# Kernel tuning notes

Measured on AMD Instinct MI355X. Metric: run time of the kernel, lower is better.

## Reference

```python
import jax, jax.numpy as jnp
import numpy as np

B, T, D_IN = 32, 1024, 80
SHAPES = (512, 512, 256)
WIN = 2          # delta window
H = 256          # LSTM hidden units (per direction)
LSTM_IN = SHAPES[-1] * 3


def setup_inputs() -> dict:
    key = jax.random.key(0)
    ks = jax.random.split(key, 20)
    inp = {}
    inp["x"] = jax.random.normal(ks[0], (B, T, D_IN), dtype=jnp.float32)
    lens = jax.random.randint(ks[1], (B,), T // 2, T + 1)
    inp["x_lengths"] = lens.at[0].set(T)  # ensure max length == T (static output shape)
    dims = (D_IN,) + SHAPES
    for i in range(len(SHAPES)):
        s = 1.0 / np.sqrt(dims[i])
        inp[f"enc_W{i}"] = jax.random.uniform(ks[2 + i], (dims[i + 1], dims[i]), minval=-s, maxval=s, dtype=jnp.float32)
        inp[f"enc_b{i}"] = jax.random.uniform(ks[5 + i], (dims[i + 1],), minval=-s, maxval=s, dtype=jnp.float32)
    s = 1.0 / np.sqrt(H)
    for d, name in enumerate(("f", "b")):
        inp[f"W_ih_{name}"] = jax.random.uniform(ks[8 + 4 * d], (4 * H, LSTM_IN), minval=-s, maxval=s, dtype=jnp.float32)
        inp[f"W_hh_{name}"] = jax.random.uniform(ks[9 + 4 * d], (4 * H, H), minval=-s, maxval=s, dtype=jnp.float32)
        inp[f"b_ih_{name}"] = jax.random.uniform(ks[10 + 4 * d], (4 * H,), minval=-s, maxval=s, dtype=jnp.float32)
        inp[f"b_hh_{name}"] = jax.random.uniform(ks[11 + 4 * d], (4 * H,), minval=-s, maxval=s, dtype=jnp.float32)
    # init_hidden() in torch uses randn; fix it here as deterministic inputs. [2 dirs, B, H]
    inp["h0"] = jax.random.normal(ks[16], (2, B, H), dtype=jnp.float32)
    inp["c0"] = jax.random.normal(ks[17], (2, B, H), dtype=jnp.float32)
    return inp


def _deltas(x, w):
    # edge-replicated window, z[:,t] = sum_j (y[t+w+j]-y[t+w-j])/(2j)
    Tt = x.shape[1]
    y = jnp.concatenate([jnp.repeat(x[:, :1], w, axis=1), x, jnp.repeat(x[:, -1:], w, axis=1)], axis=1)
    z = jnp.zeros_like(x)
    for j in range(1, w + 1):
        z = z + (y[:, w + j:w + j + Tt] - y[:, w - j:w - j + Tt]) / (2.0 * j)
    return z


def _lstm(xs, h0, c0, Wih, Whh, b):
    # xs: [T, B, F] -> hs: [T, B, H]; torch gate order i,f,g,o
    def step(carry, xt):
        h, c = carry
        g = xt @ Wih.T + h @ Whh.T + b
        i, f, gg, o = jnp.split(g, 4, axis=-1)
        c = jax.nn.sigmoid(f) * c + jax.nn.sigmoid(i) * jnp.tanh(gg)
        h = jax.nn.sigmoid(o) * jnp.tanh(c)
        return (h, c), h
    _, hs = jax.lax.scan(step, (h0, c0), xs)
    return hs


def _forward(x, x_lengths, enc_W0, enc_b0, enc_W1, enc_b1, enc_W2, enc_b2,
             W_ih_f, W_hh_f, b_ih_f, b_hh_f, W_ih_b, W_hh_b, b_ih_b, b_hh_b, h0, c0):
    # MLP encoder with ReLU after every layer
    h = x
    for Wm, bm in ((enc_W0, enc_b0), (enc_W1, enc_b1), (enc_W2, enc_b2)):
        h = jax.nn.relu(h @ Wm.T + bm)
    d1 = _deltas(h, WIN)
    d2 = _deltas(d1, WIN)
    feat = jnp.concatenate([h, d1, d2], axis=2)  # [B, T, 3*shapes[-1]]
    # sort by length descending (pack_padded_sequence)
    order = jnp.argsort(-x_lengths)
    lens = x_lengths[order]
    feat = feat[order]
    t_idx = jnp.arange(T)
    # forward direction
    hf = _lstm(jnp.swapaxes(feat, 0, 1), h0[0], c0[0], W_ih_f, W_hh_f, b_ih_f + b_hh_f)
    hf = jnp.swapaxes(hf, 0, 1)  # [B, T, H]
    # backward direction: reverse valid part of each sequence (packed semantics)
    rev = jnp.clip(lens[:, None] - 1 - t_idx[None, :], 0, T - 1)  # [B, T]
    x_rev = jnp.take_along_axis(feat, rev[:, :, None], axis=1)
    hb = _lstm(jnp.swapaxes(x_rev, 0, 1), h0[1], c0[1], W_ih_b, W_hh_b, b_ih_b + b_hh_b)
    hb = jnp.take_along_axis(jnp.swapaxes(hb, 0, 1), rev[:, :, None], axis=1)
    # pad_packed_sequence zeros out padded steps
    mask = (t_idx[None, :] < lens[:, None])[:, :, None]
    out = jnp.where(mask, jnp.concatenate([hf, hb], axis=2), 0.0)
    return out, order


def reference(x, x_lengths, enc_W0, enc_b0, enc_W1, enc_b1, enc_W2, enc_b2,
              W_ih_f, W_hh_f, b_ih_f, b_hh_f, W_ih_b, W_hh_b, b_ih_b, b_hh_b, h0, c0):
    return _forward(x, x_lengths, enc_W0, enc_b0, enc_W1, enc_b1, enc_W2, enc_b2,
                    W_ih_f, W_hh_f, b_ih_f, b_hh_f, W_ih_b, W_hh_b, b_ih_b, b_hh_b, h0, c0)
```

## Files before the change

### kernel.cpp

```cpp
#include <hip/hip_runtime.h>
#include <cstdint>
#include <cstddef>

#define B_SZ 32
#define T_SZ 1024
#define DIN  80
#define H3   256
#define FEAT 768
#define G4   1024
#define HH   256

typedef __attribute__((ext_vector_type(8))) short short8;
typedef __attribute__((ext_vector_type(4))) float f32x4;
typedef __attribute__((ext_vector_type(8))) int v8i;

__device__ inline float bf2f(unsigned short u) {
    return __uint_as_float(((unsigned int)u) << 16);
}
__device__ inline unsigned short f2bf(float f) {
    unsigned int u = __float_as_uint(f);
    u += 0x7fffu + ((u >> 16) & 1u);
    return (unsigned short)(u >> 16);
}
#define LOG2E 1.4426950408889634f
__device__ inline float sigm(float x) {
    return __builtin_amdgcn_rcpf(1.f + __builtin_amdgcn_exp2f(x * -LOG2E));
}
__device__ inline float tanh_f(float x) {
    return fmaf(2.f, __builtin_amdgcn_rcpf(1.f + __builtin_amdgcn_exp2f(x * (-2.f * LOG2E))), -1.f);
}

__device__ inline void gld16(const void* g, void* l) {
    __builtin_amdgcn_global_load_lds(
        (const __attribute__((address_space(1))) unsigned int*)g,
        (__attribute__((address_space(3))) unsigned int*)l, 16, 0, 0);
}

__device__ inline void cvt_seg(const float* __restrict__ s, unsigned short* __restrict__ d,
                               int n4, int i, int stride) {
    for (int k = i; k < n4; k += stride) {
        float4 f = ((const float4*)(const void*)s)[k];
        ushort4 u;
        u.x = f2bf(f.x); u.y = f2bf(f.y); u.z = f2bf(f.z); u.w = f2bf(f.w);
        ((ushort4*)(void*)d)[k] = u;
    }
}

__global__ void k_cvtw(const float* __restrict__ x,  unsigned short* __restrict__ xbf,
                       const float* __restrict__ s0, unsigned short* __restrict__ d0,
                       const float* __restrict__ s1, unsigned short* __restrict__ d1,
                       const float* __restrict__ s2, unsigned short* __restrict__ d2,
                       const float* __restrict__ s3, unsigned short* __restrict__ d3,
                       const float* __restrict__ s4, unsigned short* __restrict__ d4,
                       const float* __restrict__ bihf, const float* __restrict__ bhhf,
                       const float* __restrict__ bihb, const float* __restrict__ bhhb,
                       float* __restrict__ bsum,
                       const int* __restrict__ lens, int* __restrict__ order,
                       int* __restrict__ lens_sorted, float* __restrict__ out_order,
                       const float* __restrict__ Whhf, const float* __restrict__ Whhb,
                       unsigned char* __restrict__ wfrag) {
    int i = blockIdx.x * 256 + threadIdx.x;
    int stride = gridDim.x * 256;
    cvt_seg(x,  xbf, 655360, i, stride);
    cvt_seg(s0, d0, 10240,  i, stride);
    cvt_seg(s1, d1, 65536,  i, stride);
    cvt_seg(s2, d2, 32768,  i, stride);
    cvt_seg(s3, d3, 196608, i, stride);
    cvt_seg(s4, d4, 196608, i, stride);
    if (i < 2048)
        bsum[i] = (i < 1024) ? (bihf[i] + bhhf[i]) : (bihb[i - 1024] + bhhb[i - 1024]);
    if (i < B_SZ) {
        int lb = lens[i];
        int r = 0;
        for (int j = 0; j < B_SZ; ++j) {
            int lj = lens[j];
            if (lj > lb || (lj == lb && j < i)) ++r;
        }
        order[r] = i;
        lens_sorted[r] = lb;
        out_order[r] = (float)i;
    }
    if (i < 32768) {
        int t = i;
        int dir = t >> 14;
        t &= 16383;
        const float* Whh = dir ? Whhb : Whhf;
        unsigned char* d = wfrag + (size_t)dir * 262144;
        int lane = t & 63, hf = (t >> 6) & 1, kc = (t >> 7) & 1, nt = t >> 8;
        int n = nt * 16 + (lane & 15);
        int k0 = kc * 128 + (lane >> 4) * 32 + hf * 16;
        const float* p = Whh + (size_t)n * 256 + k0;
        unsigned int o[4];
        #pragma unroll
        for (int q = 0; q < 4; ++q) {
            float4 f = *(const float4*)(const void*)(p + 4 * q);
            o[q] = (__builtin_amdgcn_cvt_pk_fp8_f32(f.x, f.y, 0, false) & 0xffff)
                 | (__builtin_amdgcn_cvt_pk_fp8_f32(f.z, f.w, 0, false) << 16);
        }
        int slot = (nt * 2 + kc) * 64 + lane;
        *(uint4*)(void*)(d + (size_t)slot * 32 + hf * 16) = make_uint4(o[0], o[1], o[2], o[3]);
    }
}

__global__ void k_ztail(const int* __restrict__ lens_sorted, float* __restrict__ out) {
    int t = blockIdx.x, bs = blockIdx.y;
    if (t < lens_sorted[bs]) return;
    float4* p = (float4*)(out + ((size_t)bs * T_SZ + t) * 512);
    p[threadIdx.x] = make_float4(0.f, 0.f, 0.f, 0.f);
}

__global__ __launch_bounds__(256) void k_gemm(
    const unsigned short* __restrict__ A, const unsigned short* __restrict__ Bw,
    const float* __restrict__ bias,
    unsigned short* __restrict__ C, int M, int N, int K, int relu)
{
    int tid  = threadIdx.x;
    int lane = tid & 63;
    int wave = tid >> 6;
    int waveM = wave >> 1, waveN = wave & 1;
    int l16  = lane & 15;
    int quad = lane >> 4;
    int mBase = blockIdx.x * 32 + waveM * 16;
    int nBase = blockIdx.y * 128 + waveN * 64;

    const unsigned short* pA  = A  + (size_t)(mBase + l16) * K + quad * 8;
    const unsigned short* pB0 = Bw + (size_t)(nBase +  0 + l16) * K + quad * 8;
    const unsigned short* pB1 = Bw + (size_t)(nBase + 16 + l16) * K + quad * 8;
    const unsigned short* pB2 = Bw + (size_t)(nBase + 32 + l16) * K + quad * 8;
    const unsigned short* pB3 = Bw + (size_t)(nBase + 48 + l16) * K + quad * 8;

    const short8 z8 = {0, 0, 0, 0, 0, 0, 0, 0};
    f32x4 acc0 = {0.f, 0.f, 0.f, 0.f};
    f32x4 acc1 = acc0, acc2 = acc0, acc3 = acc0;

    for (int k0 = 0; k0 < K; k0 += 32) {
        bool ok = (k0 + quad * 8) < K;
        short8 av  = ok ? *(const short8*)(const void*)(pA  + k0) : z8;
        short8 bv0 = ok ? *(const short8*)(const void*)(pB0 + k0) : z8;
        short8 bv1 = ok ? *(const short8*)(const void*)(pB1 + k0) : z8;
        short8 bv2 = ok ? *(const short8*)(const void*)(pB2 + k0) : z8;
        short8 bv3 = ok ? *(const short8*)(const void*)(pB3 + k0) : z8;
        acc0 = __builtin_amdgcn_mfma_f32_16x16x32_bf16(av, bv0, acc0, 0, 0, 0);
        acc1 = __builtin_amdgcn_mfma_f32_16x16x32_bf16(av, bv1, acc1, 0, 0, 0);
        acc2 = __builtin_amdgcn_mfma_f32_16x16x32_bf16(av, bv2, acc2, 0, 0, 0);
        acc3 = __builtin_amdgcn_mfma_f32_16x16x32_bf16(av, bv3, acc3, 0, 0, 0);
    }

    int rowD = mBase + quad * 4;
    #pragma unroll
    for (int nt = 0; nt < 4; ++nt) {
        int col = nBase + nt * 16 + l16;
        float bsum = bias ? bias[col] : 0.f;
        f32x4 a = (nt == 0) ? acc0 : (nt == 1) ? acc1 : (nt == 2) ? acc2 : acc3;
        #pragma unroll
        for (int r = 0; r < 4; ++r) {
            float v = a[r] + bsum;
            if (relu) v = v > 0.f ? v : 0.f;
            C[(size_t)(rowD + r) * N + col] = f2bf(v);
        }
    }
}

__global__ __launch_bounds__(256) void k_gemm_t(
    const unsigned short* __restrict__ A, const unsigned short* __restrict__ Bw,
    const float* __restrict__ bias,
    unsigned short* __restrict__ C, unsigned short* __restrict__ C2,
    int N, int K, int ldc, int relu)
{
    __shared__ unsigned short lA[2][128 * 32];
    __shared__ unsigned short lB[2][128 * 32];
    int tid  = threadIdx.x;
    int lane = tid & 63;
    int wave = tid >> 6;
    int l16  = lane & 15, quad = lane >> 4;
    int wm = wave >> 1, wn = wave & 1;
    size_t mBase = (size_t)blockIdx.y * 128;
    size_t nBase = (size_t)blockIdx.x * 128;

    int c0 = tid, c1 = tid + 256;
    const unsigned short* sA0 = A  + (mBase + (c0 >> 2)) * K + (c0 & 3) * 8;
    const unsigned short* sA1 = A  + (mBase + (c1 >> 2)) * K + (c1 & 3) * 8;
    const unsigned short* sB0 = Bw + (nBase + (c0 >> 2)) * K + (c0 & 3) * 8;
    const unsigned short* sB1 = Bw + (nBase + (c1 >> 2)) * K + (c1 & 3) * 8;

    f32x4 acc[4][4];
    #pragma unroll
    for (int i = 0; i < 4; ++i)
        #pragma unroll
        for (int j = 0; j < 4; ++j) acc[i][j] = (f32x4){0.f, 0.f, 0.f, 0.f};

    int roffA = (wm * 64 + l16) * 32 + quad * 8;
    int roffB = (wn * 64 + l16) * 32 + quad * 8;

    auto STAGE = [&](int b, int k0) {
        gld16(sA0 + k0, lA[b] + c0 * 8);
        gld16(sA1 + k0, lA[b] + c1 * 8);
        gld16(sB0 + k0, lB[b] + c0 * 8);
        gld16(sB1 + k0, lB[b] + c1 * 8);
    };

    STAGE(0, 0);
    __syncthreads();
    int cur = 0;
    for (int k0 = 0; k0 < K; k0 += 32) {
        if (k0 + 32 < K) STAGE(cur ^ 1, k0 + 32);
        const unsigned short* la = lA[cur] + roffA;
        const unsigned short* lb = lB[cur] + roffB;
        short8 af[4], bf[4];
        #pragma unroll
        for (int i = 0; i < 4; ++i) {
            af[i] = *(const short8*)(const void*)(la + i * 16 * 32);
            bf[i] = *(const short8*)(const void*)(lb + i * 16 * 32);
        }
        #pragma unroll
        for (int i = 0; i < 4; ++i)
            #pragma unroll
            for (int j = 0; j < 4; ++j)
                acc[i][j] = __builtin_amdgcn_mfma_f32_16x16x32_bf16(af[i], bf[j], acc[i][j], 0, 0, 0);
        __syncthreads();
        cur ^= 1;
    }

    #pragma unroll
    for (int j = 0; j < 4; ++j) {
        int colg = (int)nBase + wn * 64 + j * 16 + l16;
        float bsum = bias[colg];
        unsigned short* dst = C;
        int cg = colg;
        if (C2 && colg >= 1024) { dst = C2; cg = colg - 1024; }
        #pragma unroll
        for (int i = 0; i < 4; ++i) {
            int row = (int)mBase + wm * 64 + i * 16 + quad * 4;
            #pragma unroll
            for (int r = 0; r < 4; ++r) {
                float v = acc[i][j][r] + bsum;
                if (relu) v = v > 0.f ? v : 0.f;
                dst[(size_t)(row + r) * ldc + cg] = f2bf(v);
            }
        }
    }
}

__global__ void k_deltas(const unsigned short* __restrict__ hbuf, const int* __restrict__ order,
                         unsigned short* __restrict__ feat)
{
    int blk = blockIdx.x;
    int bs = blk >> 8, t0 = (blk & 255) << 2;
    int c  = threadIdx.x;
    int b  = order[bs];
    const unsigned short* hb = hbuf + (size_t)b * T_SZ * H3 + c;

    unsigned short raw[12];
    float hv[12];
    #pragma unroll
    for (int d = 0; d < 12; ++d) {
        int tt = t0 - 4 + d;
        tt = tt < 0 ? 0 : (tt > T_SZ - 1 ? T_SZ - 1 : tt);
        raw[d] = hb[(size_t)tt * H3];
        hv[d] = bf2f(raw[d]);
    }
    float d1v[8];
    #pragma unroll
    for (int j = 0; j < 8; ++j)
        d1v[j] = (hv[j + 3] - hv[j + 1]) * 0.5f + (hv[j + 4] - hv[j]) * 0.25f;

    #pragma unroll
    for (int r = 0; r < 4; ++r) {
        int t = t0 + r;
        int p1 = t + 1 > T_SZ - 1 ? T_SZ - 1 : t + 1;
        int m1 = t - 1 < 0 ? 0 : t - 1;
        int p2 = t + 2 > T_SZ - 1 ? T_SZ - 1 : t + 2;
        int m2 = t - 2 < 0 ? 0 : t - 2;
        float d2 = (d1v[p1 - t0 + 2] - d1v[m1 - t0 + 2]) * 0.5f
                 + (d1v[p2 - t0 + 2] - d1v[m2 - t0 + 2]) * 0.25f;
        size_t fb = ((size_t)(bs << 10) + t) * FEAT;
        feat[fb + c]       = raw[4 + r];
        feat[fb + 256 + c] = f2bf(d1v[r + 2]);
        feat[fb + 512 + c] = f2bf(d2);
    }
}

__global__ __launch_bounds__(1024, 4) void k_lstm_fp8(
    const unsigned short* __restrict__ g3f, const unsigned short* __restrict__ g3b,
    const unsigned char* __restrict__ wfrag8,
    const float* __restrict__ h0, const float* __restrict__ c0,
    const int* __restrict__ lens_sorted, float* __restrict__ out)
{
    int rq = blockIdx.x, dir = blockIdx.y;
    const unsigned short* g3 = (dir ? g3b : g3f) + (size_t)rq * 4194304;
    const unsigned char* wsrc = wfrag8 + (size_t)dir * 262144;

    __shared__ __align__(16) unsigned char hA[2][4096];

    int tid = threadIdx.x;
    int w = tid >> 6, lane = tid & 63;
    int l16 = lane & 15, quad = lane >> 4;

    v8i regB[4][2];
    #pragma unroll
    for (int gb = 0; gb < 4; ++gb)
        #pragma unroll
        for (int kc = 0; kc < 2; ++kc) {
            int nt = gb * 16 + w;
            regB[gb][kc] = *(const v8i*)(const void*)
                (wsrc + ((size_t)((nt * 2 + kc) * 64 + lane)) * 32);
        }

    for (int i = tid; i < 2048; i += 1024) ((unsigned int*)(void*)hA)[i] = 0;
    __syncthreads();
    {
        int b = tid >> 8, c = tid & 255;
        float hv = h0[(size_t)dir * B_SZ * HH + (size_t)(rq * 4 + b) * HH + c];
        hA[0][(c >> 7) * 2048 + (((c >> 5) & 3) * 16 + 4 * b) * 32 + (c & 31)] =
            (unsigned char)(__builtin_amdgcn_cvt_pk_fp8_f32(hv, hv, 0, false) & 0xff);
    }

    int grow = rq * 4 + quad;
    int elen = lens_sorted[grow];
    int maxlen = lens_sorted[rq * 4];
    int col = w * 16 + l16;
    float c2 = c0[(size_t)dir * B_SZ * HH + (size_t)grow * HH + col];
    int woff = (col >> 7) * 2048 + (((col >> 5) & 3) * 16 + 4 * quad) * 32 + (col & 31);

    int tr0 = dir ? (elen - 1) : 0;
    int gstep = dir ? -1024 : 1024;
    int ostep = dir ? -512 : 512;
    const unsigned short* gp = g3 + ((size_t)quad << 20) + col + (size_t)tr0 * 1024;
    float* op = out + (size_t)grow * T_SZ * 512 + dir * HH + col + (size_t)tr0 * 512;

    unsigned short gI = gp[0], gF = gp[256], gG = gp[512], gO = gp[768];
    gp += gstep;

    f32x4 acc[4];
    #pragma unroll
    for (int gb = 0; gb < 4; ++gb) acc[gb] = (f32x4){0.f, 0.f, 0.f, 0.f};
    __syncthreads();

    for (int s = 0; s < maxlen; ++s) {
        const unsigned char* Ab = hA[s & 1];
        v8i a0 = *(const v8i*)(const void*)(Ab + lane * 32);
        v8i a1 = *(const v8i*)(const void*)(Ab + 2048 + lane * 32);

        unsigned short nI = gp[0], nF = gp[256], nG = gp[512], nO = gp[768];
        gp += gstep;

        acc[0][0] = bf2f(gI);
        acc[1][0] = bf2f(gF);
        acc[2][0] = bf2f(gG);
        acc[3][0] = bf2f(gO);
        #pragma unroll
        for (int gb = 0; gb < 4; ++gb)
            acc[gb] = __builtin_amdgcn_mfma_scale_f32_16x16x128_f8f6f4(
                a0, regB[gb][0], acc[gb], 0, 0, 0, 0x7F7F7F7F, 0, 0x7F7F7F7F);
        #pragma unroll
        for (int gb = 0; gb < 4; ++gb)
            acc[gb] = __builtin_amdgcn_mfma_scale_f32_16x16x128_f8f6f4(
                a1, regB[gb][1], acc[gb], 0, 0, 0, 0x7F7F7F7F, 0, 0x7F7F7F7F);

        c2 = sigm(acc[1][0]) * c2 + sigm(acc[0][0]) * tanh_f(acc[2][0]);
        float tc = tanh_f(c2);
        float hv = sigm(acc[3][0]) * tc;

        hA[(s + 1) & 1][woff] =
            (unsigned char)(__builtin_amdgcn_cvt_pk_fp8_f32(hv, hv, 0, false) & 0xff);
        if (s < elen) *op = hv;
        op += ostep;
        gI = nI; gF = nF; gG = nG; gO = nO;
        asm volatile("s_waitcnt lgkmcnt(0)" ::: "memory");
        __builtin_amdgcn_s_barrier();
    }
}

#define OFF_XBF    ((size_t)0)
#define OFF_A0     ((size_t)5242880)
#define OFF_A1     ((size_t)38797312)
#define OFF_HBUF   ((size_t)72351744)
#define OFF_FEAT   ((size_t)89128960)
#define OFF_GF     OFF_A0
#define OFF_GB     ((size_t)139460608)
#define OFF_W0     ((size_t)206569472)
#define OFF_W1     ((size_t)206651392)
#define OFF_W2     ((size_t)207175680)
#define OFF_WIHF   ((size_t)207437824)
#define OFF_WIHB   ((size_t)209010688)
#define OFF_WFRAG  ((size_t)210583552)
#define OFF_BSUM   ((size_t)211107840)
#define OFF_ORDER  ((size_t)212680704)
#define OFF_LENS   ((size_t)212680832)

extern "C" void kernel_launch(void* const* d_in, const int* in_sizes, int n_in,
                              void* d_out, int out_size, void* d_ws, size_t ws_size,
                              hipStream_t stream)
{
    const float* x    = (const float*)d_in[0];
    const int*   xlen = (const int*)d_in[1];
    const float* eW0  = (const float*)d_in[2];
    const float* eb0  = (const float*)d_in[3];
    const float* eW1  = (const float*)d_in[4];
    const float* eb1  = (const float*)d_in[5];
    const float* eW2  = (const float*)d_in[6];
    const float* eb2  = (const float*)d_in[7];
    const float* Wihf = (const float*)d_in[8];
    const float* Whhf = (const float*)d_in[9];
    const float* bihf = (const float*)d_in[10];
    const float* bhhf = (const float*)d_in[11];
    const float* Wihb = (const float*)d_in[12];
    const float* Whhb = (const float*)d_in[13];
    const float* bihb = (const float*)d_in[14];
    const float* bhhb = (const float*)d_in[15];
    const float* h0   = (const float*)d_in[16];
    const float* c0   = (const float*)d_in[17];
    float* out = (float*)d_out;

    char* ws = (char*)d_ws;
    unsigned short* xbf    = (unsigned short*)(ws + OFF_XBF);
    unsigned short* a0     = (unsigned short*)(ws + OFF_A0);
    unsigned short* a1     = (unsigned short*)(ws + OFF_A1);
    unsigned short* hbuf   = (unsigned short*)(ws + OFF_HBUF);
    unsigned short* feat   = (unsigned short*)(ws + OFF_FEAT);
    unsigned short* gatesF = (unsigned short*)(ws + OFF_GF);
    unsigned short* gatesB = (unsigned short*)(ws + OFF_GB);
    unsigned short* w0     = (unsigned short*)(ws + OFF_W0);
    unsigned short* w1     = (unsigned short*)(ws + OFF_W1);
    unsigned short* w2     = (unsigned short*)(ws + OFF_W2);
    unsigned short* wihf   = (unsigned short*)(ws + OFF_WIHF);
    unsigned short* wihb   = (unsigned short*)(ws + OFF_WIHB);
    unsigned char*  wfrag8 = (unsigned char*)(ws + OFF_WFRAG);
    float* bsum            = (float*)(ws + OFF_BSUM);
    int* order             = (int*)(ws + OFF_ORDER);
    int* lens_sorted       = (int*)(ws + OFF_LENS);

    k_cvtw<<<1024, 256, 0, stream>>>(x, xbf, eW0, w0, eW1, w1, eW2, w2,
                                     Wihf, wihf, Wihb, wihb,
                                     bihf, bhhf, bihb, bhhb, bsum,
                                     xlen, order, lens_sorted,
                                     out + (size_t)B_SZ * T_SZ * 512,
                                     Whhf, Whhb, wfrag8);
    k_ztail<<<dim3(T_SZ, B_SZ), 128, 0, stream>>>(lens_sorted, out);

    k_gemm<<<dim3(1024, 4), 256, 0, stream>>>(xbf, w0, eb0, a0, 32768, 512, 80, 1);
    k_gemm_t<<<dim3(4, 256), 256, 0, stream>>>(a0, w1, eb1, a1,   nullptr, 512, 512, 512, 1);
    k_gemm_t<<<dim3(2, 256), 256, 0, stream>>>(a1, w2, eb2, hbuf, nullptr, 256, 512, 256, 1);

    k_deltas<<<8192, 256, 0, stream>>>(hbuf, order, feat);

    k_gemm_t<<<dim3(16, 256), 256, 0, stream>>>(feat, wihf, bsum, gatesF, gatesB,
                                                2048, 768, 1024, 0);

    k_lstm_fp8<<<dim3(8, 2), 1024, 0, stream>>>(gatesF, gatesB, wfrag8, h0, c0,
                                                lens_sorted, out);
}
```

Before: 1.098 ms.

## Fuse input-gate GEMM into LSTM kernel with per-chunk counters to overlap

Result: slower. 1.740 ms (+58.5%).

```diff
diff --git a/kernel.cpp b/kernel.cpp
--- a/kernel.cpp
+++ b/kernel.cpp
@@ -58,7 +58,8 @@
                        const int* __restrict__ lens, int* __restrict__ order,
                        int* __restrict__ lens_sorted, float* __restrict__ out_order,
                        const float* __restrict__ Whhf, const float* __restrict__ Whhb,
-                       unsigned char* __restrict__ wfrag) {
+                       unsigned char* __restrict__ wfrag,
+                       unsigned int* __restrict__ cnt) {
     int i = blockIdx.x * 256 + threadIdx.x;
     int stride = gridDim.x * 256;
     cvt_seg(x,  xbf, 655360, i, stride);
@@ -69,6 +70,7 @@
     cvt_seg(s4, d4, 196608, i, stride);
     if (i < 2048)
         bsum[i] = (i < 1024) ? (bihf[i] + bhhf[i]) : (bihb[i - 1024] + bhhb[i - 1024]);
+    if (i < 256) cnt[i] = 0u;
     if (i < B_SZ) {
         int lb = lens[i];
         int r = 0;
@@ -164,8 +166,7 @@
 __global__ __launch_bounds__(256) void k_gemm_t(
     const unsigned short* __restrict__ A, const unsigned short* __restrict__ Bw,
     const float* __restrict__ bias,
-    unsigned short* __restrict__ C, unsigned short* __restrict__ C2,
-    int N, int K, int ldc, int relu)
+    unsigned short* __restrict__ C, int N, int K, int relu)
 {
     __shared__ unsigned short lA[2][128 * 32];
     __shared__ unsigned short lB[2][128 * 32];
@@ -225,9 +226,6 @@
     for (int j = 0; j < 4; ++j) {
         int colg = (int)nBase + wn * 64 + j * 16 + l16;
         float bsum = bias[colg];
-        unsigned short* dst = C;
-        int cg = colg;
-        if (C2 && colg >= 1024) { dst = C2; cg = colg - 1024; }
         #pragma unroll
         for (int i = 0; i < 4; ++i) {
             int row = (int)mBase + wm * 64 + i * 16 + quad * 4;
@@ -235,7 +233,7 @@
             for (int r = 0; r < 4; ++r) {
                 float v = acc[i][j][r] + bsum;
                 if (relu) v = v > 0.f ? v : 0.f;
-                dst[(size_t)(row + r) * ldc + cg] = f2bf(v);
+                C[(size_t)(row + r) * N + colg] = f2bf(v);
             }
         }
     }
@@ -280,19 +278,106 @@
     }
 }
 
-__global__ __launch_bounds__(1024, 4) void k_lstm_fp8(
-    const unsigned short* __restrict__ g3f, const unsigned short* __restrict__ g3b,
+__global__ __launch_bounds__(1024, 1) void k_fused(
+    const unsigned short* __restrict__ feat, const unsigned short* __restrict__ wih,
+    const float* __restrict__ bsum,
+    unsigned short* __restrict__ gatesF, unsigned short* __restrict__ gatesB,
     const unsigned char* __restrict__ wfrag8,
     const float* __restrict__ h0, const float* __restrict__ c0,
-    const int* __restrict__ lens_sorted, float* __restrict__ out)
+    const int* __restrict__ lens_sorted, float* __restrict__ out,
+    unsigned int* __restrict__ cnt)
 {
-    int rq = blockIdx.x, dir = blockIdx.y;
-    const unsigned short* g3 = (dir ? g3b : g3f) + (size_t)rq * 4194304;
+    __shared__ __align__(16) unsigned char hA[2][4096];
+    __shared__ unsigned short lds[4][2][2][4096];
+
+    int tid = threadIdx.x;
+
+    if (blockIdx.x >= 16) {
+        int gi   = (blockIdx.x - 16) * 4 + (tid >> 8);
+        int utid = tid & 255;
+        int u    = tid >> 8;
+        int ci = gi >> 9;
+        int chunk = (ci & 1) ? (ci >> 1) : (7 - (ci >> 1));
+        int r = gi & 511;
+        int bs = r >> 4;
+        int ntile = r & 15;
+        size_t mBase = ((size_t)bs << 10) + ((size_t)chunk << 7);
+        size_t nBase = (size_t)ntile << 7;
+        const int K = 768;
+
+        int lane = utid & 63, wave = utid >> 6;
+        int l16 = lane & 15, quad = lane >> 4;
+        int wm = wave >> 1, wn = wave & 1;
+
+        int c0i = utid, c1i = utid + 256;
+        const unsigned short* sA0 = feat + (mBase + (c0i >> 2)) * K + (c0i & 3) * 8;
+        const unsigned short* sA1 = feat + (mBase + (c1i >> 2)) * K + (c1i & 3) * 8;
+        const unsigned short* sB0 = wih  + (nBase + (c0i >> 2)) * K + (c0i & 3) * 8;
+        const unsigned short* sB1 = wih  + (nBase + (c1i >> 2)) * K + (c1i & 3) * 8;
+
+        f32x4 acc[4][4];
+        #pragma unroll
+        for (int i = 0; i < 4; ++i)
+            #pragma unroll
+            for (int j = 0; j < 4; ++j) acc[i][j] = (f32x4){0.f, 0.f, 0.f, 0.f};
+
+        int roffA = (wm * 64 + l16) * 32 + quad * 8;
+        int roffB = (wn * 64 + l16) * 32 + quad * 8;
+
+        auto STAGE = [&](int b, int k0) {
+            gld16(sA0 + k0, &lds[u][0][b][0] + c0i * 8);
+            gld16(sA1 + k0, &lds[u][0][b][0] + c1i * 8);
+            gld16(sB0 + k0, &lds[u][1][b][0] + c0i * 8);
+            gld16(sB1 + k0, &lds[u][1][b][0] + c1i * 8);
+        };
+
+        STAGE(0, 0);
+        __syncthreads();
+        int cur = 0;
+        for (int k0 = 0; k0 < K; k0 += 32) {
+            if (k0 + 32 < K) STAGE(cur ^ 1, k0 + 32);
+            const unsigned short* la = &lds[u][0][cur][0] + roffA;
+            const unsigned short* lb = &lds[u][1][cur][0] + roffB;
+            short8 af[4], bf[4];
+            #pragma unroll
+            for (int i = 0; i < 4; ++i) {
+                af[i] = *(const short8*)(const void*)(la + i * 16 * 32);
+                bf[i] = *(const short8*)(const void*)(lb + i * 16 * 32);
+            }
+            #pragma unroll
+            for (int i = 0; i < 4; ++i)
+                #pragma unroll
+                for (int j = 0; j < 4; ++j)
+                    acc[i][j] = __builtin_amdgcn_mfma_f32_16x16x32_bf16(af[i], bf[j], acc[i][j], 0, 0, 0);
+            __syncthreads();
+            cur ^= 1;
+        }
+
+        #pragma unroll
+        for (int j = 0; j < 4; ++j) {
+            int colg = (int)nBase + wn * 64 + j * 16 + l16;
+            float bb = bsum[colg];
+            unsigned short* dst = gatesF;
+            int cg = colg;
+            if (colg >= 1024) { dst = gatesB; cg = colg - 1024; }
+            #pragma unroll
+            for (int i = 0; i < 4; ++i) {
+                int row = (int)mBase + wm * 64 + i * 16 + quad * 4;
+                #pragma unroll
+                for (int rr = 0; rr < 4; ++rr)
+                    dst[(size_t)(row + rr) * 1024 + cg] = f2bf(acc[i][j][rr] + bb);
+            }
+        }
+        __threadfence();
+        __syncthreads();
+        if (utid == 0) atomicAdd(&cnt[(bs << 3) + chunk], 1u);
+        return;
+    }
+
+    int rq = blockIdx.x & 7, dir = blockIdx.x >> 3;
+    const unsigned short* g3 = (dir ? gatesB : gatesF) + (size_t)rq * 4194304;
     const unsigned char* wsrc = wfrag8 + (size_t)dir * 262144;
 
-    __shared__ __align__(16) unsigned char hA[2][4096];
-
-    int tid = threadIdx.x;
     int w = tid >> 6, lane = tid & 63;
     int l16 = lane & 15, quad = lane >> 4;
 
@@ -325,11 +410,28 @@
     int tr0 = dir ? (elen - 1) : 0;
     int gstep = dir ? -1024 : 1024;
     int ostep = dir ? -512 : 512;
+    int tstep = dir ? -1 : 1;
     const unsigned short* gp = g3 + ((size_t)quad << 20) + col + (size_t)tr0 * 1024;
     float* op = out + (size_t)grow * T_SZ * 512 + dir * HH + col + (size_t)tr0 * 512;
 
+    int cur_ch = -1;
+    unsigned int cbase = (unsigned int)(grow << 3);
+    auto waitc = [&](int t) {
+        if ((unsigned)t < 1024u) {
+            int ch = t >> 7;
+            if (ch != cur_ch) {
+                while (__hip_atomic_load(&cnt[cbase + (unsigned)ch], __ATOMIC_ACQUIRE,
+                                         __HIP_MEMORY_SCOPE_AGENT) < 16u)
+                    __builtin_amdgcn_s_sleep(8);
+                cur_ch = ch;
+            }
+        }
+    };
+
+    waitc(tr0);
     unsigned short gI = gp[0], gF = gp[256], gG = gp[512], gO = gp[768];
     gp += gstep;
+    int tpf = tr0;
 
     f32x4 acc[4];
     #pragma unroll
@@ -341,6 +443,8 @@
         v8i a0 = *(const v8i*)(const void*)(Ab + lane * 32);
         v8i a1 = *(const v8i*)(const void*)(Ab + 2048 + lane * 32);
 
+        tpf += tstep;
+        waitc(tpf);
         unsigned short nI = gp[0], nF = gp[256], nG = gp[512], nO = gp[768];
         gp += gstep;
 
@@ -387,6 +491,7 @@
 #define OFF_BSUM   ((size_t)211107840)
 #define OFF_ORDER  ((size_t)212680704)
 #define OFF_LENS   ((size_t)212680832)
+#define OFF_CNT    ((size_t)212680960)
 
 extern "C" void kernel_launch(void* const* d_in, const int* in_sizes, int n_in,
                               void* d_out, int out_size, void* d_ws, size_t ws_size,
@@ -429,24 +534,22 @@
     float* bsum            = (float*)(ws + OFF_BSUM);
     int* order             = (int*)(ws + OFF_ORDER);
     int* lens_sorted       = (int*)(ws + OFF_LENS);
+    unsigned int* cnt      = (unsigned int*)(ws + OFF_CNT);
 
     k_cvtw<<<1024, 256, 0, stream>>>(x, xbf, eW0, w0, eW1, w1, eW2, w2,
                                      Wihf, wihf, Wihb, wihb,
                                      bihf, bhhf, bihb, bhhb, bsum,
                                      xlen, order, lens_sorted,
                                      out + (size_t)B_SZ * T_SZ * 512,
-                                     Whhf, Whhb, wfrag8);
+                                     Whhf, Whhb, wfrag8, cnt);
     k_ztail<<<dim3(T_SZ, B_SZ), 128, 0, stream>>>(lens_sorted, out);
 
     k_gemm<<<dim3(1024, 4), 256, 0, stream>>>(xbf, w0, eb0, a0, 32768, 512, 80, 1);
-    k_gemm_t<<<dim3(4, 256), 256, 0, stream>>>(a0, w1, eb1, a1,   nullptr, 512, 512, 512, 1);
-    k_gemm_t<<<dim3(2, 256), 256, 0, stream>>>(a1, w2, eb2, hbuf, nullptr, 256, 512, 256, 1);
+    k_gemm_t<<<dim3(4, 256), 256, 0, stream>>>(a0, w1, eb1, a1,   512, 512, 1);
+    k_gemm_t<<<dim3(2, 256), 256, 0, stream>>>(a1, w2, eb2, hbuf, 256, 512, 1);
 
     k_deltas<<<8192, 256, 0, stream>>>(hbuf, order, feat);
 
-    k_gemm_t<<<dim3(16, 256), 256, 0, stream>>>(feat, wihf, bsum, gatesF, gatesB,
-                                                2048, 768, 1024, 0);
-
-    k_lstm_fp8<<<dim3(8, 2), 1024, 0, stream>>>(gatesF, gatesB, wfrag8, h0, c0,
-                                                lens_sorted, out);
-}
+    k_fused<<<1040, 1024, 0, stream>>>(feat, wihf, bsum, gatesF, gatesB,
+                                       wfrag8, h0, c0, lens_sorted, out, cnt);
+}
```
